# Optimization experiments

Measured on AMD Instinct MI355X. Metric: run time of the kernel, lower is better.

Reference implementation:

```python
import jax, jax.numpy as jnp
import numpy as np

EPS = 1e-5  # InstanceNorm2d default eps


def _branch(emb, Wq, K, Vt, Wo, kv_size):
    # emb: [b,n,c], Wq: [h,c,c] (nn.Linear weight, y = x @ W^T)
    # Qt: [b,h,c,n] = stack_h(emb @ Wq[h]^T).transpose(-1,-2)
    Qt = jnp.einsum('bnc,hdc->bhdn', emb, Wq)
    scores = jnp.einsum('bhdn,bhnk->bhdk', Qt, K) / jnp.sqrt(jnp.float32(kv_size))
    # InstanceNorm2d over heads channel: normalize each [c,kv] map per (b,h), no affine
    m = scores.mean(axis=(-2, -1), keepdims=True)
    v = scores.var(axis=(-2, -1), keepdims=True)
    scores = (scores - m) * jax.lax.rsqrt(v + EPS)
    probs = jax.nn.softmax(scores, axis=-1)            # [b,h,c,kv]
    ctx = jnp.einsum('bhdk,bhkn->bhdn', probs, Vt)     # [b,h,c,n]
    ctx = ctx.mean(axis=1).transpose(0, 2, 1)          # mean over heads -> [b,n,c]
    return ctx @ Wo.T


def setup_inputs() -> dict:
    key = jax.random.key(0)
    ks = jax.random.split(key, 15)
    B, N, H, KV = 16, 196, 4, 960
    C = [64, 128, 256, 512]
    inp = {}
    for i, c in enumerate(C):
        inp[f'emb{i+1}'] = jax.random.normal(ks[i], (B, N, c), jnp.float32)
    inp['emb_all'] = jax.random.normal(ks[4], (B, N, KV), jnp.float32)
    for i, c in enumerate(C):
        inp[f'Wq{i+1}'] = jax.random.normal(ks[5 + i], (H, c, c), jnp.float32) / np.sqrt(c)
    inp['Wk'] = jax.random.normal(ks[9], (H, KV, KV), jnp.float32) / np.sqrt(KV)
    inp['Wv'] = jax.random.normal(ks[10], (H, KV, KV), jnp.float32) / np.sqrt(KV)
    for i, c in enumerate(C):
        inp[f'Wo{i+1}'] = jax.random.normal(ks[11 + i], (c, c), jnp.float32) / np.sqrt(c)
    return inp


def reference(emb1, emb2, emb3, emb4, emb_all,
              Wq1, Wq2, Wq3, Wq4, Wk, Wv, Wo1, Wo2, Wo3, Wo4):
    KV = emb_all.shape[-1]
    # per-head shared K and V: [b,h,n,kv]; Vt = V.transpose(-1,-2): [b,h,kv,n]
    K = jnp.einsum('bnk,hok->bhno', emb_all, Wk)
    Vt = jnp.einsum('bnk,hok->bhon', emb_all, Wv)
    O1 = _branch(emb1, Wq1, K, Vt, Wo1, KV)
    O2 = _branch(emb2, Wq2, K, Vt, Wo2, KV)
    O3 = _branch(emb3, Wq3, K, Vt, Wo3, KV)
    O4 = _branch(emb4, Wq4, K, Vt, Wo4, KV)
    return (O1, O2, O3, O4)
```

## Files before the change

kernel.cpp:

```cpp
#include <hip/hip_runtime.h>
#include <hip/hip_fp16.h>
#include <math.h>

#define BB 16
#define NP 196
#define HH 4
#define KVD 960
#define KP 224
#define LDK 200

typedef __attribute__((ext_vector_type(8))) short s8v;
typedef __attribute__((ext_vector_type(8))) unsigned short u8v;
typedef __attribute__((ext_vector_type(4))) unsigned short u4v;
typedef __attribute__((ext_vector_type(4))) float f4v;

static inline int divup(int a, int b){ return (a+b-1)/b; }
static inline int imin(int a, int b){ return a < b ? a : b; }

__device__ __forceinline__ unsigned short bf16r(float x){
    unsigned int u = __float_as_uint(x);
    u += 0x7fffu + ((u >> 16) & 1u);
    return (unsigned short)(u >> 16);
}
__device__ __forceinline__ float bf16f(unsigned short h){
    return __uint_as_float(((unsigned int)h) << 16);
}

__device__ __forceinline__ void gload16(const unsigned short* g, unsigned short* l){
    __builtin_amdgcn_global_load_lds(
        (const __attribute__((address_space(1))) void*)g,
        (__attribute__((address_space(3))) void*)l, 16, 0, 0);
}

struct DecTable {
    const float* src[15];
    unsigned short* dh[15];
    unsigned short* dl[15];
    long n4[15];
};

__global__ __launch_bounds__(256)
void decomp_all(DecTable T)
{
    int seg = blockIdx.y;
    const float* x = T.src[seg];
    unsigned short* hi = T.dh[seg];
    unsigned short* lo = T.dl[seg];
    long n4 = T.n4[seg];
    for (long i = (long)blockIdx.x * 256 + threadIdx.x; i < n4; i += (long)gridDim.x * 256) {
        float4 v = ((const float4*)x)[i];
        float a[4] = {v.x, v.y, v.z, v.w};
        u4v h, l;
#pragma unroll
        for (int e = 0; e < 4; e++) {
            unsigned short hb = bf16r(a[e]);
            h[e] = hb;
            l[e] = bf16r(a[e] - bf16f(hb));
        }
        *(u4v*)(hi + i * 4) = h;
        *(u4v*)(lo + i * 4) = l;
    }
}

template<int OUTK, int STATS>
__global__ __launch_bounds__(256)
void gemm_split(const unsigned short* __restrict__ Ah, const unsigned short* __restrict__ Al,
                const unsigned short* __restrict__ Bh, const unsigned short* __restrict__ Bl,
                float* __restrict__ Cf, unsigned short* __restrict__ Ch,
                unsigned short* __restrict__ Cl, double* __restrict__ part,
                int M, int Nn, int Kk, int ldA, int ldB, int ldC,
                long sAb, long sAh_, long sBb, long sBh_, long sCb, long sCh_,
                int Hdiv, float alpha)
{
    __shared__ u8v AsV[128 * 8];
    __shared__ u8v BsV[128 * 8];
    unsigned short* As = (unsigned short*)AsV;
    unsigned short* Bs = (unsigned short*)BsV;

    int z  = blockIdx.z;
    int bb = z / Hdiv, hz = z - bb * Hdiv;
    const unsigned short* gah = Ah + (long)bb * sAb + (long)hz * sAh_;
    const unsigned short* gal = Al + (long)bb * sAb + (long)hz * sAh_;
    const unsigned short* gbh = Bh + (long)bb * sBb + (long)hz * sBh_;
    const unsigned short* gbl = Bl + (long)bb * sBb + (long)hz * sBh_;
    long coff = (long)bb * sCb + (long)hz * sCh_;

    int t = threadIdx.x;
    int m0 = blockIdx.y * 128, n0 = blockIdx.x * 128;
    int wave = t >> 6, lane = t & 63;
    int wm = wave >> 1, wn = wave & 1;
    int lr = lane & 15, lk = lane >> 4;

    int ls   = (lane & 7) ^ (lane >> 3);
    int comp = ls >> 2;
    int chnk = ls & 3;
    const unsigned short* gA = comp ? gal : gah;
    const unsigned short* gB = comp ? gbl : gbh;
    const unsigned short* aptr[4];
    const unsigned short* bptr[4];
#pragma unroll
    for (int j = 0; j < 4; j++) {
        int ra = m0 + wave * 32 + j * 8 + (lane >> 3);
        ra = (ra < M) ? ra : (M - 1);
        aptr[j] = gA + (long)ra * ldA + chnk * 8;
        int rb = n0 + wave * 32 + j * 8 + (lane >> 3);
        rb = (rb < Nn) ? rb : (Nn - 1);
        bptr[j] = gB + (long)rb * ldB + chnk * 8;
    }

    f4v acc[4][4];
#pragma unroll
    for (int i = 0; i < 4; i++)
#pragma unroll
        for (int j = 0; j < 4; j++) acc[i][j] = (f4v){0.f, 0.f, 0.f, 0.f};

    int nkt = Kk >> 5;
    for (int kt = 0; kt < nkt; ++kt) {
        int k0 = kt << 5;
#pragma unroll
        for (int j = 0; j < 4; j++) {
            gload16(aptr[j] + k0, As + (wave * 4 + j) * 512);
            gload16(bptr[j] + k0, Bs + (wave * 4 + j) * 512);
        }
        __syncthreads();

        s8v afh[4], afl[4], bfh[4], bfl[4];
#pragma unroll
        for (int i = 0; i < 4; i++) {
            int rw = wm * 64 + i * 16 + lr;
            afh[i] = *(const s8v*)&As[rw * 64 + ((lk ^ (rw & 7)) << 3)];
            afl[i] = *(const s8v*)&As[rw * 64 + (((lk + 4) ^ (rw & 7)) << 3)];
            int cw = wn * 64 + i * 16 + lr;
            bfh[i] = *(const s8v*)&Bs[cw * 64 + ((lk ^ (cw & 7)) << 3)];
            bfl[i] = *(const s8v*)&Bs[cw * 64 + (((lk + 4) ^ (cw & 7)) << 3)];
        }
#pragma unroll
        for (int i = 0; i < 4; i++)
#pragma unroll
            for (int j = 0; j < 4; j++) {
                acc[i][j] = __builtin_amdgcn_mfma_f32_16x16x32_bf16(afh[i], bfh[j], acc[i][j], 0, 0, 0);
                acc[i][j] = __builtin_amdgcn_mfma_f32_16x16x32_bf16(afl[i], bfh[j], acc[i][j], 0, 0, 0);
                acc[i][j] = __builtin_amdgcn_mfma_f32_16x16x32_bf16(afh[i], bfl[j], acc[i][j], 0, 0, 0);
            }
        __syncthreads();
    }

    float s1 = 0.f, s2 = 0.f;
#pragma unroll
    for (int i = 0; i < 4; i++)
#pragma unroll
        for (int j = 0; j < 4; j++)
#pragma unroll
            for (int r = 0; r < 4; r++) {
                int gr = m0 + wm * 64 + i * 16 + lk * 4 + r;
                int gc = n0 + wn * 64 + j * 16 + lr;
                if (gr < M) {
                    if (gc < Nn) {
                        float v = acc[i][j][r] * alpha;
                        if (STATS) { s1 += v; s2 += v * v; }
                        if (OUTK == 1) {
                            unsigned short hb = bf16r(v);
                            Ch[coff + (long)gr * ldC + gc] = hb;
                            Cl[coff + (long)gr * ldC + gc] = bf16r(v - bf16f(hb));
                        } else if (OUTK == 2) {
                            __half hh = __float2half(v);
                            unsigned short us;
                            __builtin_memcpy(&us, &hh, 2);
                            Ch[coff + (long)gr * ldC + gc] = us;
                        } else {
                            Cf[coff + (long)gr * ldC + gc] = v;
                        }
                    } else if (OUTK == 1 && gc < ldC) {
                        Ch[coff + (long)gr * ldC + gc] = 0;
                        Cl[coff + (long)gr * ldC + gc] = 0;
                    }
                }
            }

    if (STATS) {
        double* sh = (double*)AsV;
        sh[t] = (double)s1; sh[256 + t] = (double)s2;
        __syncthreads();
        for (int o = 128; o > 0; o >>= 1) {
            if (t < o) { sh[t] += sh[t + o]; sh[256 + t] += sh[256 + t + o]; }
            __syncthreads();
        }
        if (t == 0) {
            int slot = blockIdx.x + (int)gridDim.x * blockIdx.y;
            part[(long)z * 64 + slot * 2 + 0] = sh[0];
            part[(long)z * 64 + slot * 2 + 1] = sh[256];
        }
    }
}

__global__ __launch_bounds__(256)
void pv_fused(const unsigned short* __restrict__ Sb, const unsigned short* __restrict__ Vh,
              const unsigned short* __restrict__ Vl, const double* __restrict__ part,
              float* __restrict__ Cb, int c, int m0, int nslot)
{
    __shared__ unsigned short As[64 * 64];
    __shared__ unsigned short Bs[224 * 64];
    __shared__ float Zlds[64];
    __shared__ float bc2[2];

    int z  = blockIdx.z;
    int gm = m0 + z;
    int my0 = blockIdx.y * 64;

    int t = threadIdx.x;
    int wave = t >> 6, lane = t & 63;
    int wm = wave >> 1, wn = wave & 1;
    int lr = lane & 15, lk = lane >> 4;

    if (t == 0) {
        const double* pp = part + (long)gm * 64;
        double su = 0.0, sq = 0.0;
        for (int q = 0; q < nslot; q++) { su += pp[q * 2]; sq += pp[q * 2 + 1]; }
        float inv_e = 1.0f / (float)(c * KVD);
        float mean = (float)(su * (double)inv_e);
        float var  = (float)(sq * (double)inv_e) - mean * mean;
        float is   = rsqrtf(var + 1e-5f);
        bc2[0] = is; bc2[1] = -mean * is;
    }
    __syncthreads();
    float is = bc2[0], dd = bc2[1];

    int arow = t >> 2, achk = t & 3;
    const unsigned short* sp = Sb + (size_t)z * c * KVD + (size_t)(my0 + arow) * KVD + achk * 8;
    unsigned short* awh = &As[arow * 64 + (( achk      ^ (arow & 7)) << 3)];
    unsigned short* awl = &As[arow * 64 + (((achk + 4) ^ (arow & 7)) << 3)];

    int ls   = (lane & 7) ^ (lane >> 3);
    int comp = ls >> 2, chnk = ls & 3;
    const unsigned short* vbase = (comp ? Vl : Vh) + (long)gm * (196L * KVD);
    const unsigned short* bptr[7];
    unsigned short* bdst[7];
#pragma unroll
    for (int q = 0; q < 7; q++) {
        int rlog = (wave * 7 + q) * 8 + (lane >> 3);
        int vrow = (rlog < NP) ? rlog : (NP - 1);
        bptr[q] = vbase + (long)vrow * KVD + chnk * 8;
        bdst[q] = &Bs[(wave * 7 + q) * 512];
    }

    f4v acc[2][7];
#pragma unroll
    for (int i = 0; i < 2; i++)
#pragma unroll
        for (int j = 0; j < 7; j++) acc[i][j] = (f4v){0.f, 0.f, 0.f, 0.f};
    float zp = 0.f;

    for (int kt = 0; kt < 30; ++kt) {
        int k0 = kt << 5;
#pragma unroll
        for (int q = 0; q < 7; q++) gload16(bptr[q] + k0, bdst[q]);

        u8v sv = *(const u8v*)(sp + k0);
        u8v hv, lv;
#pragma unroll
        for (int e = 0; e < 8; e++) {
            __half hh;
            unsigned short us = sv[e];
            __builtin_memcpy(&hh, &us, 2);
            float p = __expf(fmaf(__half2float(hh), is, dd));
            zp += p;
            unsigned short hb = bf16r(p);
            hv[e] = hb;
            lv[e] = bf16r(p - bf16f(hb));
        }
        *(u8v*)awh = hv;
        *(u8v*)awl = lv;
        __syncthreads();

        s8v afh[2], afl[2], bfh[7], bfl[7];
#pragma unroll
        for (int i = 0; i < 2; i++) {
            int ar = wm * 32 + i * 16 + lr;
            afh[i] = *(const s8v*)&As[ar * 64 + ((lk ^ (ar & 7)) << 3)];
            afl[i] = *(const s8v*)&As[ar * 64 + (((lk + 4) ^ (ar & 7)) << 3)];
        }
#pragma unroll
        for (int j = 0; j < 7; j++) {
            int br = wn * 112 + j * 16 + lr;
            bfh[j] = *(const s8v*)&Bs[br * 64 + ((lk ^ (br & 7)) << 3)];
            bfl[j] = *(const s8v*)&Bs[br * 64 + (((lk + 4) ^ (br & 7)) << 3)];
        }
#pragma unroll
        for (int i = 0; i < 2; i++)
#pragma unroll
            for (int j = 0; j < 7; j++) {
                acc[i][j] = __builtin_amdgcn_mfma_f32_16x16x32_bf16(afh[i], bfh[j], acc[i][j], 0, 0, 0);
                acc[i][j] = __builtin_amdgcn_mfma_f32_16x16x32_bf16(afl[i], bfh[j], acc[i][j], 0, 0, 0);
                acc[i][j] = __builtin_amdgcn_mfma_f32_16x16x32_bf16(afh[i], bfl[j], acc[i][j], 0, 0, 0);
            }
        __syncthreads();
    }

    zp += __shfl_xor(zp, 1);
    zp += __shfl_xor(zp, 2);
    if ((t & 3) == 0) Zlds[arow] = zp;
    __syncthreads();

    float rz[2][4];
#pragma unroll
    for (int i = 0; i < 2; i++)
#pragma unroll
        for (int r = 0; r < 4; r++)
            rz[i][r] = 1.0f / Zlds[wm * 32 + i * 16 + lk * 4 + r];

    float* co = Cb + (size_t)gm * c * NP;
#pragma unroll
    for (int i = 0; i < 2; i++)
#pragma unroll
        for (int j = 0; j < 7; j++)
#pragma unroll
            for (int r = 0; r < 4; r++) {
                int grl = wm * 32 + i * 16 + lk * 4 + r;
                int gc  = wn * 112 + j * 16 + lr;
                if (gc < NP)
                    co[(size_t)(my0 + grl) * NP + gc] = acc[i][j][r] * rz[i][r];
            }
}

__global__ __launch_bounds__(256)
void mean_t_kernel(const float* __restrict__ Cb, unsigned short* __restrict__ Mh,
                   unsigned short* __restrict__ Ml, int c)
{
    int b  = blockIdx.z;
    int n0 = blockIdx.x * 32;
    int d0 = blockIdx.y * 32;
    __shared__ float tile[32][33];
    int tx = threadIdx.x & 31;
    int ty = threadIdx.x >> 5;
#pragma unroll
    for (int i = 0; i < 4; i++) {
        int d = d0 + ty + i * 8;
        int n = n0 + tx;
        float s = 0.f;
        if (n < NP) {
#pragma unroll
            for (int h = 0; h < HH; h++)
                s += Cb[(((long)(b * HH + h)) * c + d) * NP + n];
        }
        tile[ty + i * 8][tx] = 0.25f * s;
    }
    __syncthreads();
#pragma unroll
    for (int i = 0; i < 4; i++) {
        int n = n0 + ty + i * 8;
        int d = d0 + tx;
        if (n < NP) {
            float val = tile[tx][ty + i * 8];
            long idx = ((long)b * NP + n) * c + d;
            unsigned short hb = bf16r(val);
            Mh[idx] = hb;
            Ml[idx] = bf16r(val - bf16f(hb));
        }
    }
}

extern "C" void kernel_launch(void* const* d_in, const int* in_sizes, int n_in,
                              void* d_out, int out_size, void* d_ws, size_t ws_size,
                              hipStream_t stream)
{
    const float* embf[4] = {(const float*)d_in[0], (const float*)d_in[1],
                            (const float*)d_in[2], (const float*)d_in[3]};
    const float* emb_all = (const float*)d_in[4];
    const float* Wq[4]   = {(const float*)d_in[5], (const float*)d_in[6],
                            (const float*)d_in[7], (const float*)d_in[8]};
    const float* Wk = (const float*)d_in[9];
    const float* Wv = (const float*)d_in[10];
    const float* Wo[4]   = {(const float*)d_in[11], (const float*)d_in[12],
                            (const float*)d_in[13], (const float*)d_in[14]};
    float* out = (float*)d_out;

    const int Cc[4] = {64, 128, 256, 512};

    char* base = (char*)d_ws;
    size_t off = 0;
    auto align256 = [](size_t b) -> size_t { return (b + 255) & ~(size_t)255; };
    auto carve = [&](size_t bytes) -> void* {
        void* p = base + off;
        off += align256(bytes);
        return p;
    };

    const long NEA   = (long)BB * NP * KVD;
    const long NWKV  = (long)HH * KVD * KVD;
    const long SUMC2 = 64L*64 + 128L*128 + 256L*256 + 512L*512;

    unsigned short* wkH = (unsigned short*)carve(NWKV * 2);
    unsigned short* wkL = (unsigned short*)carve(NWKV * 2);
    unsigned short* wvH = (unsigned short*)carve(NWKV * 2);
    unsigned short* wvL = (unsigned short*)carve(NWKV * 2);
    unsigned short* wqH = (unsigned short*)carve((long)HH * SUMC2 * 2);
    unsigned short* wqL = (unsigned short*)carve((long)HH * SUMC2 * 2);
    unsigned short* woH = (unsigned short*)carve(SUMC2 * 2);
    unsigned short* woL = (unsigned short*)carve(SUMC2 * 2);
    unsigned short* eiH = (unsigned short*)carve(NEA * 2);
    unsigned short* eiL = (unsigned short*)carve(NEA * 2);
    double* part = (double*)carve(64L * 64 * 8);

    size_t fixed_off = off;
    const size_t eaBytes = 2 * align256(NEA * 2);

    auto group_bytes = [&](int gb) -> size_t {
        long nbh = (long)gb * HH;
        size_t s = 0;
        auto add = [&](size_t b){ s += align256(b); };
        add(nbh * KVD * LDK * 2 + 512); add(nbh * KVD * LDK * 2 + 512);
        add(nbh * NP * KVD * 2); add(nbh * NP * KVD * 2);
        add(nbh * 512 * KP * 2); add(nbh * 512 * KP * 2);
        add(nbh * 512 * NP * 4);
        add((long)gb * NP * 512 * 2); add((long)gb * NP * 512 * 2);
        return s;
    };

    int GB;
    bool eaChunk;
    if (fixed_off + group_bytes(16) + eaBytes + (2u << 20) <= ws_size) {
        GB = 16; eaChunk = true;
    } else {
        eaChunk = false;
        const size_t minchunk = (size_t)512 * KVD * 2 + (1u << 20);
        GB = 8;
        while (GB > 1 && fixed_off + eaBytes + group_bytes(GB) + minchunk > ws_size) GB >>= 1;
    }
    unsigned short* eaH = nullptr;
    unsigned short* eaL = nullptr;
    if (!eaChunk) {
        eaH = (unsigned short*)carve(NEA * 2);
        eaL = (unsigned short*)carve(NEA * 2);
    }
    const long NBH = (long)GB * HH;

    unsigned short* KtH = (unsigned short*)carve(NBH * KVD * LDK * 2 + 512);
    unsigned short* KtL = (unsigned short*)carve(NBH * KVD * LDK * 2 + 512);
    unsigned short* VH  = (unsigned short*)carve(NBH * NP * KVD * 2);
    unsigned short* VL  = (unsigned short*)carve(NBH * NP * KVD * 2);
    unsigned short* QtH = (unsigned short*)carve(NBH * 512 * KP * 2);
    unsigned short* QtL = (unsigned short*)carve(NBH * 512 * KP * 2);
    float*  Cb          = (float*)carve(NBH * 512 * NP * 4);
    unsigned short* MbH = (unsigned short*)carve((long)GB * NP * 512 * 2);
    unsigned short* MbL = (unsigned short*)carve((long)GB * NP * 512 * 2);

    char* chunk = base + off;
    size_t savail = (ws_size > off) ? (ws_size - off) : 0;
    if (eaChunk) {
        eaH = (unsigned short*)chunk;
        eaL = (unsigned short*)(chunk + align256(NEA * 2));
    }

    dim3 blk(256);
    const float alphaS = 1.0f / sqrtf((float)KVD);

    long eio[4], wqo[4], woo[4];
    { long eo = 0, qo = 0, oo = 0;
      for (int i = 0; i < 4; i++) {
          eio[i] = eo; eo += (long)BB * NP * Cc[i];
          wqo[i] = qo; qo += (long)HH * Cc[i] * Cc[i];
          woo[i] = oo; oo += (long)Cc[i] * Cc[i];
      } }
    {
        DecTable T;
        int k = 0;
        for (int i = 0; i < 4; i++) {
            T.src[k] = embf[i]; T.dh[k] = eiH + eio[i]; T.dl[k] = eiL + eio[i];
            T.n4[k] = ((long)BB * NP * Cc[i]) / 4; k++;
        }
        T.src[k] = emb_all; T.dh[k] = eaH; T.dl[k] = eaL; T.n4[k] = NEA / 4; k++;
        for (int i = 0; i < 4; i++) {
            T.src[k] = Wq[i]; T.dh[k] = wqH + wqo[i]; T.dl[k] = wqL + wqo[i];
            T.n4[k] = ((long)HH * Cc[i] * Cc[i]) / 4; k++;
        }
        T.src[k] = Wk; T.dh[k] = wkH; T.dl[k] = wkL; T.n4[k] = NWKV / 4; k++;
        T.src[k] = Wv; T.dh[k] = wvH; T.dl[k] = wvL; T.n4[k] = NWKV / 4; k++;
        for (int i = 0; i < 4; i++) {
            T.src[k] = Wo[i]; T.dh[k] = woH + woo[i]; T.dl[k] = woL + woo[i];
            T.n4[k] = ((long)Cc[i] * Cc[i]) / 4; k++;
        }
        decomp_all<<<dim3(512, 15, 1), blk, 0, stream>>>(T);
    }

    long obase[4];
    { long o = 0; for (int i = 0; i < 4; i++) { obase[i] = o; o += (long)BB * NP * Cc[i]; } }

    for (int g0 = 0; g0 < BB; g0 += GB) {
        const unsigned short* eaHg = eaH + (long)g0 * NP * KVD;
        const unsigned short* eaLg = eaL + (long)g0 * NP * KVD;

        gemm_split<1,0><<<dim3(2, 8, (int)NBH), blk, 0, stream>>>(
            wkH, wkL, eaHg, eaLg, nullptr, KtH, KtL, nullptr,
            KVD, NP, KVD, KVD, KVD, LDK,
            0, (long)KVD * KVD, (long)NP * KVD, 0,
            (long)HH * KVD * LDK, (long)KVD * LDK, HH, 1.0f);

        gemm_split<1,0><<<dim3(8, 2, (int)NBH), blk, 0, stream>>>(
            eaHg, eaLg, wvH, wvL, nullptr, VH, VL, nullptr,
            NP, KVD, KVD, KVD, KVD, KVD,
            (long)NP * KVD, 0, 0, (long)KVD * KVD,
            (long)HH * NP * KVD, (long)NP * KVD, HH, 1.0f);

        for (int i = 0; i < 4; i++) {
            int c = Cc[i];

            gemm_split<1,0><<<dim3(2, divup(HH * c, 128), GB), blk, 0, stream>>>(
                wqH + wqo[i], wqL + wqo[i],
                eiH + eio[i] + (long)g0 * NP * c, eiL + eio[i] + (long)g0 * NP * c,
                nullptr, QtH, QtL, nullptr,
                HH * c, NP, c, c, c, KP,
                0, 0, (long)NP * c, 0,
                (long)HH * c * KP, 0, 1, 1.0f);

            int nslot = 8 * divup(c, 128);

            size_t per = (size_t)c * KVD * 2;
            int G = (savail >= per) ? (int)(savail / per) : 1;
            if (G > (int)NBH) G = (int)NBH;
            if (G < 1) G = 1;
            unsigned short* Sb = (unsigned short*)chunk;

            for (int m0 = 0; m0 < (int)NBH; m0 += G) {
                int g = imin(G, (int)NBH - m0);
                gemm_split<2,1><<<dim3(8, divup(c, 128), g), blk, 0, stream>>>(
                    QtH + (size_t)m0 * c * KP, QtL + (size_t)m0 * c * KP,
                    KtH + (size_t)m0 * KVD * LDK, KtL + (size_t)m0 * KVD * LDK,
                    nullptr, Sb, nullptr, part + (size_t)m0 * 64,
                    c, KVD, KP, KP, LDK, KVD,
                    (long)c * KP, 0, (long)KVD * LDK, 0, (long)c * KVD, 0,
                    1, alphaS);
                pv_fused<<<dim3(1, c / 64, g), blk, 0, stream>>>(
                    Sb, VH, VL, part, Cb, c, m0, nslot);
            }
            mean_t_kernel<<<dim3(divup(NP, 32), c / 32, GB), blk, 0, stream>>>(Cb, MbH, MbL, c);
            gemm_split<0,0><<<dim3(divup(c, 128), divup(GB * NP, 128), 1), blk, 0, stream>>>(
                MbH, MbL, woH + woo[i], woL + woo[i],
                out + obase[i] + (long)g0 * NP * c, nullptr, nullptr, nullptr,
                GB * NP, c, c, c, c, c,
                0, 0, 0, 0, 0, 0, 1, 1.0f);
        }
    }
}
```

Before: 972.8 us.

## Stack all four branches' Q into one 960-row map per head and batch launches

Places each branch's Q projection at a fixed row offset in one 960-row buffer. One score GEMM and one PV kernel then cover all branches per (batch,head) group, with per-branch instance-norm statistics taken from slot ranges. The context buffer is now fp16 and sized for all 64 maps, and the mean/output projection runs once per branch after the loop. This cuts kernel launch count and small-grid underutilisation, at the cost of fp16 rounding on the context and a larger workspace.

```diff
diff --git a/kernel.cpp b/kernel.cpp
--- a/kernel.cpp
+++ b/kernel.cpp
@@ -8,6 +8,7 @@
 #define KVD 960
 #define KP 224
 #define LDK 200
+#define SM 960
 
 typedef __attribute__((ext_vector_type(8))) short s8v;
 typedef __attribute__((ext_vector_type(8))) unsigned short u8v;
@@ -187,8 +188,8 @@
         }
         if (t == 0) {
             int slot = blockIdx.x + (int)gridDim.x * blockIdx.y;
-            part[(long)z * 64 + slot * 2 + 0] = sh[0];
-            part[(long)z * 64 + slot * 2 + 1] = sh[256];
+            part[(long)z * 128 + slot * 2 + 0] = sh[0];
+            part[(long)z * 128 + slot * 2 + 1] = sh[256];
         }
     }
 }
@@ -196,7 +197,7 @@
 __global__ __launch_bounds__(256)
 void pv_fused(const unsigned short* __restrict__ Sb, const unsigned short* __restrict__ Vh,
               const unsigned short* __restrict__ Vl, const double* __restrict__ part,
-              float* __restrict__ Cb, int c, int m0, int nslot)
+              __half* __restrict__ Cb, int m0)
 {
     __shared__ unsigned short As[64 * 64];
     __shared__ unsigned short Bs[224 * 64];
@@ -213,10 +214,15 @@
     int lr = lane & 15, lk = lane >> 4;
 
     if (t == 0) {
-        const double* pp = part + (long)gm * 64;
+        int br = (my0 >= 896) ? 3 : (my0 >= 768) ? 2 : (my0 >= 512) ? 1 : 0;
+        const int by0_[4] = {0, 4, 6, 7};
+        const int nby_[4] = {4, 2, 1, 1};
+        const int cbr_[4] = {512, 256, 128, 64};
+        const double* pp = part + (long)z * 128;
         double su = 0.0, sq = 0.0;
-        for (int q = 0; q < nslot; q++) { su += pp[q * 2]; sq += pp[q * 2 + 1]; }
-        float inv_e = 1.0f / (float)(c * KVD);
+        int q0 = 8 * by0_[br], q1 = 8 * (by0_[br] + nby_[br]);
+        for (int q = q0; q < q1; q++) { su += pp[q * 2]; sq += pp[q * 2 + 1]; }
+        float inv_e = 1.0f / (float)(cbr_[br] * KVD);
         float mean = (float)(su * (double)inv_e);
         float var  = (float)(sq * (double)inv_e) - mean * mean;
         float is   = rsqrtf(var + 1e-5f);
@@ -226,13 +232,13 @@
     float is = bc2[0], dd = bc2[1];
 
     int arow = t >> 2, achk = t & 3;
-    const unsigned short* sp = Sb + (size_t)z * c * KVD + (size_t)(my0 + arow) * KVD + achk * 8;
+    const unsigned short* sp = Sb + (size_t)z * SM * KVD + (size_t)(my0 + arow) * KVD + achk * 8;
     unsigned short* awh = &As[arow * 64 + (( achk      ^ (arow & 7)) << 3)];
     unsigned short* awl = &As[arow * 64 + (((achk + 4) ^ (arow & 7)) << 3)];
 
     int ls   = (lane & 7) ^ (lane >> 3);
     int comp = ls >> 2, chnk = ls & 3;
-    const unsigned short* vbase = (comp ? Vl : Vh) + (long)gm * (196L * KVD);
+    const unsigned short* vbase = (comp ? Vl : Vh) + (long)z * (196L * KVD);
     const unsigned short* bptr[7];
     unsigned short* bdst[7];
 #pragma unroll
@@ -281,9 +287,9 @@
         }
 #pragma unroll
         for (int j = 0; j < 7; j++) {
-            int br = wn * 112 + j * 16 + lr;
-            bfh[j] = *(const s8v*)&Bs[br * 64 + ((lk ^ (br & 7)) << 3)];
-            bfl[j] = *(const s8v*)&Bs[br * 64 + (((lk + 4) ^ (br & 7)) << 3)];
+            int br2 = wn * 112 + j * 16 + lr;
+            bfh[j] = *(const s8v*)&Bs[br2 * 64 + ((lk ^ (br2 & 7)) << 3)];
+            bfl[j] = *(const s8v*)&Bs[br2 * 64 + (((lk + 4) ^ (br2 & 7)) << 3)];
         }
 #pragma unroll
         for (int i = 0; i < 2; i++)
@@ -308,7 +314,7 @@
         for (int r = 0; r < 4; r++)
             rz[i][r] = 1.0f / Zlds[wm * 32 + i * 16 + lk * 4 + r];
 
-    float* co = Cb + (size_t)gm * c * NP;
+    __half* co = Cb + (size_t)gm * SM * NP;
 #pragma unroll
     for (int i = 0; i < 2; i++)
 #pragma unroll
@@ -318,13 +324,13 @@
                 int grl = wm * 32 + i * 16 + lk * 4 + r;
                 int gc  = wn * 112 + j * 16 + lr;
                 if (gc < NP)
-                    co[(size_t)(my0 + grl) * NP + gc] = acc[i][j][r] * rz[i][r];
+                    co[(size_t)(my0 + grl) * NP + gc] = __float2half(acc[i][j][r] * rz[i][r]);
             }
 }
 
 __global__ __launch_bounds__(256)
-void mean_t_kernel(const float* __restrict__ Cb, unsigned short* __restrict__ Mh,
-                   unsigned short* __restrict__ Ml, int c)
+void mean_t_kernel(const __half* __restrict__ Cb, unsigned short* __restrict__ Mh,
+                   unsigned short* __restrict__ Ml, int c, int roff)
 {
     int b  = blockIdx.z;
     int n0 = blockIdx.x * 32;
@@ -340,7 +346,7 @@
         if (n < NP) {
 #pragma unroll
             for (int h = 0; h < HH; h++)
-                s += Cb[(((long)(b * HH + h)) * c + d) * NP + n];
+                s += __half2float(Cb[((long)(b * HH + h) * SM + roff + d) * NP + n]);
         }
         tile[ty + i * 8][tx] = 0.25f * s;
     }
@@ -374,7 +380,8 @@
                             (const float*)d_in[13], (const float*)d_in[14]};
     float* out = (float*)d_out;
 
-    const int Cc[4] = {64, 128, 256, 512};
+    const int Cc[4]   = {64, 128, 256, 512};
+    const int roff[4] = {896, 768, 512, 0};
 
     char* base = (char*)d_ws;
     size_t off = 0;
@@ -388,6 +395,7 @@
     const long NEA   = (long)BB * NP * KVD;
     const long NWKV  = (long)HH * KVD * KVD;
     const long SUMC2 = 64L*64 + 128L*128 + 256L*256 + 512L*512;
+    const long NMAP  = (long)BB * HH;
 
     unsigned short* wkH = (unsigned short*)carve(NWKV * 2);
     unsigned short* wkL = (unsigned short*)carve(NWKV * 2);
@@ -399,57 +407,42 @@
     unsigned short* woL = (unsigned short*)carve(SUMC2 * 2);
     unsigned short* eiH = (unsigned short*)carve(NEA * 2);
     unsigned short* eiL = (unsigned short*)carve(NEA * 2);
-    double* part = (double*)carve(64L * 64 * 8);
-
-    size_t fixed_off = off;
-    const size_t eaBytes = 2 * align256(NEA * 2);
-
-    auto group_bytes = [&](int gb) -> size_t {
-        long nbh = (long)gb * HH;
+    unsigned short* eaH = (unsigned short*)carve(NEA * 2);
+    unsigned short* eaL = (unsigned short*)carve(NEA * 2);
+    double* part = (double*)carve(64L * 128 * 8);
+    __half* Cb   = (__half*)carve(NMAP * SM * NP * 2);
+    unsigned short* MbH = (unsigned short*)carve((long)BB * NP * 512 * 2);
+    unsigned short* MbL = (unsigned short*)carve((long)BB * NP * 512 * 2);
+
+    size_t static_off = off;
+    size_t zavail = (ws_size > static_off) ? (ws_size - static_off) : 0;
+
+    auto chunk_bytes = [&](int g) -> size_t {
         size_t s = 0;
         auto add = [&](size_t b){ s += align256(b); };
-        add(nbh * KVD * LDK * 2 + 512); add(nbh * KVD * LDK * 2 + 512);
-        add(nbh * NP * KVD * 2); add(nbh * NP * KVD * 2);
-        add(nbh * 512 * KP * 2); add(nbh * 512 * KP * 2);
-        add(nbh * 512 * NP * 4);
-        add((long)gb * NP * 512 * 2); add((long)gb * NP * 512 * 2);
+        add((size_t)g * KVD * LDK * 2 + 512); add((size_t)g * KVD * LDK * 2 + 512);
+        add((size_t)g * NP * KVD * 2);        add((size_t)g * NP * KVD * 2);
+        add((size_t)g * SM * KP * 2);         add((size_t)g * SM * KP * 2);
+        add((size_t)g * SM * KVD * 2);
         return s;
     };
-
-    int GB;
-    bool eaChunk;
-    if (fixed_off + group_bytes(16) + eaBytes + (2u << 20) <= ws_size) {
-        GB = 16; eaChunk = true;
-    } else {
-        eaChunk = false;
-        const size_t minchunk = (size_t)512 * KVD * 2 + (1u << 20);
-        GB = 8;
-        while (GB > 1 && fixed_off + eaBytes + group_bytes(GB) + minchunk > ws_size) GB >>= 1;
-    }
-    unsigned short* eaH = nullptr;
-    unsigned short* eaL = nullptr;
-    if (!eaChunk) {
-        eaH = (unsigned short*)carve(NEA * 2);
-        eaL = (unsigned short*)carve(NEA * 2);
-    }
-    const long NBH = (long)GB * HH;
-
-    unsigned short* KtH = (unsigned short*)carve(NBH * KVD * LDK * 2 + 512);
-    unsigned short* KtL = (unsigned short*)carve(NBH * KVD * LDK * 2 + 512);
-    unsigned short* VH  = (unsigned short*)carve(NBH * NP * KVD * 2);
-    unsigned short* VL  = (unsigned short*)carve(NBH * NP * KVD * 2);
-    unsigned short* QtH = (unsigned short*)carve(NBH * 512 * KP * 2);
-    unsigned short* QtL = (unsigned short*)carve(NBH * 512 * KP * 2);
-    float*  Cb          = (float*)carve(NBH * 512 * NP * 4);
-    unsigned short* MbH = (unsigned short*)carve((long)GB * NP * 512 * 2);
-    unsigned short* MbL = (unsigned short*)carve((long)GB * NP * 512 * 2);
-
-    char* chunk = base + off;
-    size_t savail = (ws_size > off) ? (ws_size - off) : 0;
-    if (eaChunk) {
-        eaH = (unsigned short*)chunk;
-        eaL = (unsigned short*)(chunk + align256(NEA * 2));
-    }
+    int G = 64;
+    while (G > 4 && chunk_bytes(G) > zavail) G -= 4;
+
+    char* cz = base + static_off;
+    size_t co2 = 0;
+    auto czcarve = [&](size_t bytes) -> void* {
+        void* p = cz + co2;
+        co2 += align256(bytes);
+        return p;
+    };
+    unsigned short* KtH = (unsigned short*)czcarve((size_t)G * KVD * LDK * 2 + 512);
+    unsigned short* KtL = (unsigned short*)czcarve((size_t)G * KVD * LDK * 2 + 512);
+    unsigned short* VH  = (unsigned short*)czcarve((size_t)G * NP * KVD * 2);
+    unsigned short* VL  = (unsigned short*)czcarve((size_t)G * NP * KVD * 2);
+    unsigned short* QtH = (unsigned short*)czcarve((size_t)G * SM * KP * 2);
+    unsigned short* QtL = (unsigned short*)czcarve((size_t)G * SM * KP * 2);
+    unsigned short* Sb  = (unsigned short*)czcarve((size_t)G * SM * KVD * 2);
 
     dim3 blk(256);
     const float alphaS = 1.0f / sqrtf((float)KVD);
@@ -485,59 +478,54 @@
     long obase[4];
     { long o = 0; for (int i = 0; i < 4; i++) { obase[i] = o; o += (long)BB * NP * Cc[i]; } }
 
-    for (int g0 = 0; g0 < BB; g0 += GB) {
-        const unsigned short* eaHg = eaH + (long)g0 * NP * KVD;
-        const unsigned short* eaLg = eaL + (long)g0 * NP * KVD;
-
-        gemm_split<1,0><<<dim3(2, 8, (int)NBH), blk, 0, stream>>>(
-            wkH, wkL, eaHg, eaLg, nullptr, KtH, KtL, nullptr,
+    for (int m0 = 0; m0 < (int)NMAP; m0 += G) {
+        int g = imin(G, (int)NMAP - m0);
+        int b0 = m0 / HH;
+
+        gemm_split<1,0><<<dim3(2, 8, g), blk, 0, stream>>>(
+            wkH, wkL, eaH + (long)b0 * NP * KVD, eaL + (long)b0 * NP * KVD,
+            nullptr, KtH, KtL, nullptr,
             KVD, NP, KVD, KVD, KVD, LDK,
             0, (long)KVD * KVD, (long)NP * KVD, 0,
             (long)HH * KVD * LDK, (long)KVD * LDK, HH, 1.0f);
 
-        gemm_split<1,0><<<dim3(8, 2, (int)NBH), blk, 0, stream>>>(
-            eaHg, eaLg, wvH, wvL, nullptr, VH, VL, nullptr,
+        gemm_split<1,0><<<dim3(8, 2, g), blk, 0, stream>>>(
+            eaH + (long)b0 * NP * KVD, eaL + (long)b0 * NP * KVD, wvH, wvL,
+            nullptr, VH, VL, nullptr,
             NP, KVD, KVD, KVD, KVD, KVD,
             (long)NP * KVD, 0, 0, (long)KVD * KVD,
             (long)HH * NP * KVD, (long)NP * KVD, HH, 1.0f);
 
         for (int i = 0; i < 4; i++) {
             int c = Cc[i];
-
-            gemm_split<1,0><<<dim3(2, divup(HH * c, 128), GB), blk, 0, stream>>>(
+            gemm_split<1,0><<<dim3(2, divup(c, 128), g), blk, 0, stream>>>(
                 wqH + wqo[i], wqL + wqo[i],
-                eiH + eio[i] + (long)g0 * NP * c, eiL + eio[i] + (long)g0 * NP * c,
-                nullptr, QtH, QtL, nullptr,
-                HH * c, NP, c, c, c, KP,
-                0, 0, (long)NP * c, 0,
-                (long)HH * c * KP, 0, 1, 1.0f);
-
-            int nslot = 8 * divup(c, 128);
-
-            size_t per = (size_t)c * KVD * 2;
-            int G = (savail >= per) ? (int)(savail / per) : 1;
-            if (G > (int)NBH) G = (int)NBH;
-            if (G < 1) G = 1;
-            unsigned short* Sb = (unsigned short*)chunk;
-
-            for (int m0 = 0; m0 < (int)NBH; m0 += G) {
-                int g = imin(G, (int)NBH - m0);
-                gemm_split<2,1><<<dim3(8, divup(c, 128), g), blk, 0, stream>>>(
-                    QtH + (size_t)m0 * c * KP, QtL + (size_t)m0 * c * KP,
-                    KtH + (size_t)m0 * KVD * LDK, KtL + (size_t)m0 * KVD * LDK,
-                    nullptr, Sb, nullptr, part + (size_t)m0 * 64,
-                    c, KVD, KP, KP, LDK, KVD,
-                    (long)c * KP, 0, (long)KVD * LDK, 0, (long)c * KVD, 0,
-                    1, alphaS);
-                pv_fused<<<dim3(1, c / 64, g), blk, 0, stream>>>(
-                    Sb, VH, VL, part, Cb, c, m0, nslot);
-            }
-            mean_t_kernel<<<dim3(divup(NP, 32), c / 32, GB), blk, 0, stream>>>(Cb, MbH, MbL, c);
-            gemm_split<0,0><<<dim3(divup(c, 128), divup(GB * NP, 128), 1), blk, 0, stream>>>(
-                MbH, MbL, woH + woo[i], woL + woo[i],
-                out + obase[i] + (long)g0 * NP * c, nullptr, nullptr, nullptr,
-                GB * NP, c, c, c, c, c,
-                0, 0, 0, 0, 0, 0, 1, 1.0f);
-        }
-    }
-}
+                eiH + eio[i] + (long)b0 * NP * c, eiL + eio[i] + (long)b0 * NP * c,
+                nullptr, QtH + (long)roff[i] * KP, QtL + (long)roff[i] * KP, nullptr,
+                c, NP, c, c, c, KP,
+                0, (long)c * c, (long)NP * c, 0,
+                (long)HH * SM * KP, (long)SM * KP, HH, 1.0f);
+        }
+
+        gemm_split<2,1><<<dim3(8, 8, g), blk, 0, stream>>>(
+            QtH, QtL, KtH, KtL,
+            nullptr, Sb, nullptr, part,
+            SM, KVD, KP, KP, LDK, KVD,
+            (long)SM * KP, 0, (long)KVD * LDK, 0, (long)SM * KVD, 0,
+            1, alphaS);
+
+        pv_fused<<<dim3(1, SM / 64, g), blk, 0, stream>>>(
+            Sb, VH, VL, part, Cb, m0);
+    }
+
+    for (int i = 0; i < 4; i++) {
+        int c = Cc[i];
+        mean_t_kernel<<<dim3(divup(NP, 32), c / 32, BB), blk, 0, stream>>>(
+            Cb, MbH, MbL, c, roff[i]);
+        gemm_split<0,0><<<dim3(divup(c, 128), divup(BB * NP, 128), 1), blk, 0, stream>>>(
+            MbH, MbL, woH + woo[i], woL + woo[i],
+            out + obase[i], nullptr, nullptr, nullptr,
+            BB * NP, c, c, c, c, c,
+            0, 0, 0, 0, 0, 0, 1, 1.0f);
+    }
+}
```

New measurement: 918.1 us. 5.6% less time.
